# Optimization experiments

Hardware: AMD Instinct MI355X
Metric: run time of the kernel (lower is better)

The kernel has to match this reference:

```python
import jax, jax.numpy as jnp
import numpy as np

N_NODES = 256
BATCH = 262144
LIP_CONSTANT = 1.0
N_ITER = 20  # power-iteration steps for the Lipschitz (spectral) normalization


def _spectral_norm(W, n_iter=N_ITER):
    # Power iteration for the largest singular value of W.
    v = jnp.ones((W.shape[1],), W.dtype) / jnp.sqrt(jnp.asarray(W.shape[1], W.dtype))
    def body(v, _):
        u = W @ v
        u = u / (jnp.linalg.norm(u) + 1e-12)
        v = W.T @ u
        v = v / (jnp.linalg.norm(v) + 1e-12)
        return v, None
    v, _ = jax.lax.scan(body, v, None, length=n_iter)
    v = jax.lax.stop_gradient(v)
    return jnp.linalg.norm(W @ v) + 1e-12


def setup_inputs() -> dict:
    key = jax.random.key(0)
    kx, kw = jax.random.split(key)
    x = jax.random.normal(kx, (BATCH, N_NODES), dtype=jnp.float32)
    # learned weight of the square linearLipschitz layer (bias=False)
    W = jax.random.normal(kw, (N_NODES, N_NODES), dtype=jnp.float32) / jnp.sqrt(N_NODES)
    return {"x": x, "W": W}


def reference(x, W):
    # Lipschitz-constrained effective weight: W scaled so its spectral norm
    # equals lip_constant.
    W_eff = W * (LIP_CONSTANT / _spectral_norm(W))
    # Original loop: f_x[:, i] = layer(x @ U_i)[:, i] with U_i = I, U_i[i,i]=0.
    # => f_x[:, i] = sum_{j != i} x[:, j] * W_eff[i, j]
    # Collapsed: one GEMM minus the diagonal term.
    return x @ W_eff.T - x * jnp.diag(W_eff)[None, :]
```

## Files before the change

kernel.cpp:

```cpp
#include <hip/hip_runtime.h>
#include <stdint.h>

#define NN 256
#define BATCH 262144

typedef unsigned short ushort_t;
typedef __attribute__((ext_vector_type(8))) short short8_t;
typedef __attribute__((ext_vector_type(4))) float f32x4;

__device__ __forceinline__ ushort_t f2bf(float f) {
  uint32_t u = __float_as_uint(f);
  u += 0x7fffu + ((u >> 16) & 1u);
  return (ushort_t)(u >> 16);
}

__global__ __launch_bounds__(256) void gram_kernel(const float* __restrict__ W,
                                                   float* __restrict__ M) {
  int bi = blockIdx.x >> 4, bj = blockIdx.x & 15;
  int ti = threadIdx.x >> 4, tj = threadIdx.x & 15;
  int i = bi * 16 + ti, j = bj * 16 + tj;
  float acc = 0.f;
#pragma unroll 8
  for (int k = 0; k < NN; ++k) acc += W[k * NN + i] * W[k * NN + j];
  M[i * NN + j] = acc;
}

__global__ __launch_bounds__(256) void matsq_kernel(const float* __restrict__ A,
                                                    float* __restrict__ C) {
  int bi = blockIdx.x >> 4, bj = blockIdx.x & 15;
  int ti = threadIdx.x >> 4, tj = threadIdx.x & 15;
  int i = bi * 16 + ti, j = bj * 16 + tj;
  float acc = 0.f;
#pragma unroll 8
  for (int k = 0; k < NN; ++k) acc += A[i * NN + k] * A[k * NN + j];
  C[i * NN + j] = acc;
}

__global__ __launch_bounds__(1024) void power_kernel(const float* __restrict__ W,
                                                     const float* __restrict__ M,
                                                     const float* __restrict__ M4,
                                                     ushort_t* __restrict__ wz) {
  __shared__ float v_lds[NN];
  __shared__ float psum[4 * NN];
  __shared__ float red[16];
  __shared__ float scale_s;
  const int t = threadIdx.x;
  const int r = t >> 2, qc = t & 3;

  f32x4 Mreg[16];
#pragma unroll
  for (int j = 0; j < 16; ++j)
    Mreg[j] = *(const f32x4*)(M4 + r * NN + j * 16 + qc * 4);

  if (t < NN) v_lds[t] = 0.0625f;
  __syncthreads();

  for (int it = 0; it < 5; ++it) {
    float p = 0.f;
#pragma unroll
    for (int j = 0; j < 16; ++j) {
      f32x4 v4 = *(const f32x4*)(v_lds + j * 16 + qc * 4);
      p += Mreg[j].x * v4.x + Mreg[j].y * v4.y + Mreg[j].z * v4.z + Mreg[j].w * v4.w;
    }
    psum[qc * NN + r] = p;
    __syncthreads();
    if (t < NN)
      v_lds[t] = psum[t] + psum[NN + t] + psum[2 * NN + t] + psum[3 * NN + t];
    __syncthreads();
  }

  {
    float p = 0.f;
#pragma unroll
    for (int j = 0; j < 16; ++j) {
      f32x4 m4 = *(const f32x4*)(M + r * NN + j * 16 + qc * 4);
      f32x4 v4 = *(const f32x4*)(v_lds + j * 16 + qc * 4);
      p += m4.x * v4.x + m4.y * v4.y + m4.z * v4.z + m4.w * v4.w;
    }
    psum[qc * NN + r] = p;
    __syncthreads();
    float num = 0.f, den = 0.f;
    if (t < NN) {
      float y = psum[t] + psum[NN + t] + psum[2 * NN + t] + psum[3 * NN + t];
      float v = v_lds[t];
      num = v * y;
      den = v * v;
    }
#pragma unroll
    for (int off = 32; off > 0; off >>= 1) {
      num += __shfl_down(num, off);
      den += __shfl_down(den, off);
    }
    if (t < NN && (t & 63) == 0) {
      red[(t >> 6) * 2] = num;
      red[(t >> 6) * 2 + 1] = den;
    }
    __syncthreads();
    if (t == 0) {
      float n = red[0] + red[2] + red[4] + red[6];
      float d = red[1] + red[3] + red[5] + red[7];
      float sig = sqrtf(n / d) + 1e-12f;
      scale_s = 1.0f / sig;
    }
    __syncthreads();
  }
  const float scale = scale_s;

  for (int o = t; o < 8192; o += 1024) {
    int n = o >> 5;
    int koct = o & 31;
    int k0 = koct * 8;
    int kt = koct >> 2, kq = koct & 3;
    int kqs = kq ^ ((n >> 1) & 3);
    f32x4 a = *(const f32x4*)(W + n * NN + k0);
    f32x4 b = *(const f32x4*)(W + n * NN + k0 + 4);
    float f[8] = {a.x, a.y, a.z, a.w, b.x, b.y, b.z, b.w};
    short8_t pack;
#pragma unroll
    for (int e = 0; e < 8; ++e) {
      float val = (n == k0 + e) ? 0.f : f[e] * scale;
      pack[e] = (short)f2bf(val);
    }
    *(short8_t*)(wz + kt * 8192 + n * 32 + kqs * 8) = pack;
  }
}

__global__ __launch_bounds__(256, 3) void gemm_kernel(const float* __restrict__ x,
                                                      const ushort_t* __restrict__ wz,
                                                      float* __restrict__ out) {
  __shared__ __align__(16) ushort_t lsA[64 * 32];
  __shared__ __align__(16) ushort_t lsB[256 * 32];
  const int tid = threadIdx.x;
  const int wave = tid >> 6, lane = tid & 63;
  const int m0 = blockIdx.x * 64;
  const int m = lane & 15, q = lane >> 4;
  const int sw = (m >> 1) & 3;

  f32x4 acc[4][4];
  const f32x4 zero = {0.f, 0.f, 0.f, 0.f};
#pragma unroll
  for (int a = 0; a < 4; ++a)
#pragma unroll
    for (int b = 0; b < 4; ++b) acc[a][b] = zero;

  const int ar = tid >> 2;
  const int ak = tid & 3;
  const int achunk = ar * 4 + (ak ^ ((ar >> 1) & 3));
  const float* aptr = x + (m0 + ar) * NN + ak * 8;

  for (int kt = 0; kt < 8; ++kt) {
#pragma unroll
    for (int i = 0; i < 4; ++i) {
      const int cbase = i * 256 + wave * 64;
      __builtin_amdgcn_global_load_lds(
          (const __attribute__((address_space(1))) uint32_t*)(wz + kt * 8192 +
                                                              (cbase + lane) * 8),
          (__attribute__((address_space(3))) uint32_t*)(lsB + cbase * 8), 16, 0, 0);
    }
    f32x4 a0 = *(const f32x4*)(aptr + kt * 32);
    f32x4 a1 = *(const f32x4*)(aptr + kt * 32 + 4);
    short8_t av;
    av[0] = (short)f2bf(a0.x); av[1] = (short)f2bf(a0.y);
    av[2] = (short)f2bf(a0.z); av[3] = (short)f2bf(a0.w);
    av[4] = (short)f2bf(a1.x); av[5] = (short)f2bf(a1.y);
    av[6] = (short)f2bf(a1.z); av[7] = (short)f2bf(a1.w);
    *(short8_t*)(lsA + achunk * 8) = av;
    __syncthreads();

    short8_t af[4], bfrag[4];
#pragma unroll
    for (int mt = 0; mt < 4; ++mt) {
      int c = (mt * 16 + m) * 4 + (q ^ sw);
      af[mt] = *(const short8_t*)(lsA + c * 8);
    }
#pragma unroll
    for (int nt = 0; nt < 4; ++nt) {
      int c = (wave * 64 + nt * 16 + m) * 4 + (q ^ sw);
      bfrag[nt] = *(const short8_t*)(lsB + c * 8);
    }
#pragma unroll
    for (int mt = 0; mt < 4; ++mt)
#pragma unroll
      for (int nt = 0; nt < 4; ++nt)
        acc[mt][nt] = __builtin_amdgcn_mfma_f32_16x16x32_bf16(af[mt], bfrag[nt],
                                                              acc[mt][nt], 0, 0, 0);
    __syncthreads();
  }

#pragma unroll
  for (int mt = 0; mt < 4; ++mt) {
#pragma unroll
    for (int nt = 0; nt < 4; ++nt) {
      const int col = wave * 64 + nt * 16 + m;
      const int rowb = m0 + mt * 16 + q * 4;
#pragma unroll
      for (int e = 0; e < 4; ++e) out[(rowb + e) * NN + col] = acc[mt][nt][e];
    }
  }
}

extern "C" void kernel_launch(void* const* d_in, const int* in_sizes, int n_in,
                              void* d_out, int out_size, void* d_ws, size_t ws_size,
                              hipStream_t stream) {
  const float* x = (const float*)d_in[0];
  const float* W = (const float*)d_in[1];
  float* out = (float*)d_out;

  char* ws = (char*)d_ws;
  ushort_t* wz = (ushort_t*)ws;
  float* M = (float*)(ws + 131072);
  float* M2 = (float*)(ws + 131072 + 262144);
  float* M4 = (float*)(ws + 131072 + 2 * 262144);

  gram_kernel<<<256, 256, 0, stream>>>(W, M);
  matsq_kernel<<<256, 256, 0, stream>>>(M, M2);
  matsq_kernel<<<256, 256, 0, stream>>>(M2, M4);
  power_kernel<<<1, 1024, 0, stream>>>(W, M, M4, wz);
  gemm_kernel<<<BATCH / 64, 256, 0, stream>>>(x, wz, out);
}
```

Baseline: 495.8 us.

## Double-buffer LDS tiles in GEMM to overlap loads with MFMA

Splits the A and B shared-memory tiles into two buffers and prefetches the next k-tile (x values into registers, W via global_load_lds) while MFMAs run on the current tile. This halves the barriers per iteration and is meant to hide global-load latency behind compute. In exchange the kernel uses twice the LDS (about 40KB per block), which may limit how many blocks fit per CU under the launch bound of 3, and the loop is fully unrolled, which can raise register pressure.

```diff
diff --git a/kernel.cpp b/kernel.cpp
--- a/kernel.cpp
+++ b/kernel.cpp
@@ -128,8 +128,8 @@
 __global__ __launch_bounds__(256, 3) void gemm_kernel(const float* __restrict__ x,
                                                       const ushort_t* __restrict__ wz,
                                                       float* __restrict__ out) {
-  __shared__ __align__(16) ushort_t lsA[64 * 32];
-  __shared__ __align__(16) ushort_t lsB[256 * 32];
+  __shared__ __align__(16) ushort_t lsA[2][64 * 32];
+  __shared__ __align__(16) ushort_t lsB[2][256 * 32];
   const int tid = threadIdx.x;
   const int wave = tid >> 6, lane = tid & 63;
   const int m0 = blockIdx.x * 64;
@@ -148,35 +148,54 @@
   const int achunk = ar * 4 + (ak ^ ((ar >> 1) & 3));
   const float* aptr = x + (m0 + ar) * NN + ak * 8;
 
-  for (int kt = 0; kt < 8; ++kt) {
+  {
+    f32x4 c0 = *(const f32x4*)(aptr);
+    f32x4 c1 = *(const f32x4*)(aptr + 4);
 #pragma unroll
     for (int i = 0; i < 4; ++i) {
       const int cbase = i * 256 + wave * 64;
       __builtin_amdgcn_global_load_lds(
-          (const __attribute__((address_space(1))) uint32_t*)(wz + kt * 8192 +
-                                                              (cbase + lane) * 8),
-          (__attribute__((address_space(3))) uint32_t*)(lsB + cbase * 8), 16, 0, 0);
-    }
-    f32x4 a0 = *(const f32x4*)(aptr + kt * 32);
-    f32x4 a1 = *(const f32x4*)(aptr + kt * 32 + 4);
+          (const __attribute__((address_space(1))) uint32_t*)(wz + (cbase + lane) * 8),
+          (__attribute__((address_space(3))) uint32_t*)(&lsB[0][cbase * 8]), 16, 0, 0);
+    }
     short8_t av;
-    av[0] = (short)f2bf(a0.x); av[1] = (short)f2bf(a0.y);
-    av[2] = (short)f2bf(a0.z); av[3] = (short)f2bf(a0.w);
-    av[4] = (short)f2bf(a1.x); av[5] = (short)f2bf(a1.y);
-    av[6] = (short)f2bf(a1.z); av[7] = (short)f2bf(a1.w);
-    *(short8_t*)(lsA + achunk * 8) = av;
-    __syncthreads();
+    av[0] = (short)f2bf(c0.x); av[1] = (short)f2bf(c0.y);
+    av[2] = (short)f2bf(c0.z); av[3] = (short)f2bf(c0.w);
+    av[4] = (short)f2bf(c1.x); av[5] = (short)f2bf(c1.y);
+    av[6] = (short)f2bf(c1.z); av[7] = (short)f2bf(c1.w);
+    *(short8_t*)(&lsA[0][achunk * 8]) = av;
+    __syncthreads();
+  }
+
+#pragma unroll
+  for (int kt = 0; kt < 8; ++kt) {
+    const int cur = kt & 1, nxt = cur ^ 1;
+
+    f32x4 c0, c1;
+    if (kt < 7) {
+      c0 = *(const f32x4*)(aptr + (kt + 1) * 32);
+      c1 = *(const f32x4*)(aptr + (kt + 1) * 32 + 4);
+#pragma unroll
+      for (int i = 0; i < 4; ++i) {
+        const int cbase = i * 256 + wave * 64;
+        __builtin_amdgcn_global_load_lds(
+            (const __attribute__((address_space(1))) uint32_t*)(wz + (kt + 1) * 8192 +
+                                                                (cbase + lane) * 8),
+            (__attribute__((address_space(3))) uint32_t*)(&lsB[nxt][cbase * 8]), 16, 0,
+            0);
+      }
+    }
 
     short8_t af[4], bfrag[4];
 #pragma unroll
     for (int mt = 0; mt < 4; ++mt) {
       int c = (mt * 16 + m) * 4 + (q ^ sw);
-      af[mt] = *(const short8_t*)(lsA + c * 8);
+      af[mt] = *(const short8_t*)(&lsA[cur][c * 8]);
     }
 #pragma unroll
     for (int nt = 0; nt < 4; ++nt) {
       int c = (wave * 64 + nt * 16 + m) * 4 + (q ^ sw);
-      bfrag[nt] = *(const short8_t*)(lsB + c * 8);
+      bfrag[nt] = *(const short8_t*)(&lsB[cur][c * 8]);
     }
 #pragma unroll
     for (int mt = 0; mt < 4; ++mt)
@@ -184,7 +203,16 @@
       for (int nt = 0; nt < 4; ++nt)
         acc[mt][nt] = __builtin_amdgcn_mfma_f32_16x16x32_bf16(af[mt], bfrag[nt],
                                                               acc[mt][nt], 0, 0, 0);
-    __syncthreads();
+
+    if (kt < 7) {
+      short8_t av;
+      av[0] = (short)f2bf(c0.x); av[1] = (short)f2bf(c0.y);
+      av[2] = (short)f2bf(c0.z); av[3] = (short)f2bf(c0.w);
+      av[4] = (short)f2bf(c1.x); av[5] = (short)f2bf(c1.y);
+      av[6] = (short)f2bf(c1.z); av[7] = (short)f2bf(c1.w);
+      *(short8_t*)(&lsA[nxt][achunk * 8]) = av;
+      __syncthreads();
+    }
   }
 
 #pragma unroll
```

After: 495.3 us. About the same (-0.1%).
